# Performance work log

Measured on AMD Instinct MI355X. Metric: run time of the kernel, lower is better.

## Reference

```python
import jax, jax.numpy as jnp
import numpy as np

D_MODEL = 1024
NUM_HEADS = 16
DILATION = 2
SEG = 2048


def setup_inputs() -> dict:
    key = jax.random.key(0)
    k1, k2, k3, k4, k5 = jax.random.split(key, 5)
    B, S, D = 2, 8192, D_MODEL
    scale = 1.0 / np.sqrt(D)
    x = jax.random.normal(k1, (B, S, D), dtype=jnp.float32)
    wqkv = jax.random.normal(k2, (D, 3 * D), dtype=jnp.float32) * scale
    bqkv = jnp.zeros((3 * D,), dtype=jnp.float32)
    wo = jax.random.normal(k3, (D, D), dtype=jnp.float32) * scale
    bo = jnp.zeros((D,), dtype=jnp.float32)
    return {"x": x, "wqkv": wqkv, "bqkv": bqkv, "wo": wo, "bo": bo}


def reference(x, wqkv, bqkv, wo, bo):
    B, S, D = x.shape
    H = NUM_HEADS
    hd = D // H
    # segment reshape + dilated strided slice: [B, N, L, D]
    xs = x.reshape(B, -1, SEG, D)[:, :, ::DILATION, :]
    Bn, N, L, _ = xs.shape
    # fused QKV projection
    qkv = xs @ wqkv + bqkv                       # [B, N, L, 3D]
    q, k, v = jnp.split(qkv, 3, axis=-1)
    q = q.reshape(B, N, L, H, hd)
    k = k.reshape(B, N, L, H, hd)
    v = v.reshape(B, N, L, H, hd)
    scale = 1.0 / jnp.sqrt(jnp.asarray(hd, dtype=x.dtype))
    scores = jnp.einsum("bnqhd,bnkhd->bnhqk", q, k) * scale
    attn = jax.nn.softmax(scores, axis=-1)
    out = jnp.einsum("bnhqk,bnkhd->bnqhd", attn, v).reshape(B, N, L, D)
    out = out @ wo + bo                          # out projection
    return out.reshape(B, N * L, D)
```

## Files before the change

kernel.cpp:

```cpp
#include <hip/hip_runtime.h>
#include <hip/hip_bf16.h>
#include <stdint.h>

typedef __attribute__((ext_vector_type(8))) short short8;
typedef __attribute__((ext_vector_type(4))) float float4v;
typedef __attribute__((ext_vector_type(4))) unsigned int uint4v;
typedef unsigned short u16;

#if __has_builtin(__builtin_amdgcn_exp2f)
#define EXP2F(x) __builtin_amdgcn_exp2f(x)
#else
#define EXP2F(x) __expf(0.69314718056f * (x))
#endif

__device__ __forceinline__ u16 f2b(float f) {
    union { __hip_bfloat16 b; u16 u; } cv;
    cv.b = __float2bfloat16(f);
    return cv.u;
}

#define GLD16(g, l) __builtin_amdgcn_global_load_lds( \
    (const __attribute__((address_space(1))) void*)(g), \
    (__attribute__((address_space(3))) void*)(l), 16, 0, 0)

__global__ void convert_x(const float* __restrict__ x, u16* __restrict__ xb) {
    int id = blockIdx.x * 256 + threadIdx.x;
    int row = id >> 8;
    int c4 = id & 255;
    const float4* src = reinterpret_cast<const float4*>(x + (size_t)(2 * row) * 1024) + c4;
    float4 v = *src;
    ushort4 o;
    o.x = f2b(v.x); o.y = f2b(v.y); o.z = f2b(v.z); o.w = f2b(v.w);
    *(reinterpret_cast<ushort4*>(xb + (size_t)row * 1024) + c4) = o;
}

__global__ void transpose_convert(const float* __restrict__ in, u16* __restrict__ out,
                                  int K, int N) {
    __shared__ float tile[32][33];
    int n0 = blockIdx.x * 32, k0 = blockIdx.y * 32;
    int tx = threadIdx.x, ty = threadIdx.y;
#pragma unroll
    for (int i = 0; i < 4; i++)
        tile[ty + i * 8][tx] = in[(size_t)(k0 + ty + i * 8) * N + n0 + tx];
    __syncthreads();
#pragma unroll
    for (int i = 0; i < 4; i++)
        out[(size_t)(n0 + ty + i * 8) * K + k0 + tx] = f2b(tile[tx][ty + i * 8]);
}

template <int MODE>
__global__ __launch_bounds__(256) void gemm_bt(
    const u16* __restrict__ A, const u16* __restrict__ BT,
    const float* __restrict__ bias,
    float* __restrict__ Cf, u16* __restrict__ Cqk, u16* __restrict__ Cvt,
    int M, int N, int K) {
    __shared__ u16 As[128 * 64];
    __shared__ u16 Bs[128 * 64];
    const int tid = threadIdx.x;
    const int w = tid >> 6, l = tid & 63;
    const int q = l >> 4, c = l & 15;
    const int m0 = blockIdx.y * 128, n0 = blockIdx.x * 128;
    const int wm = (w >> 1) * 64, wn = (w & 1) * 64;

    const int srow = w * 8 + (l >> 3);
    const int scol = ((l & 7) ^ (srow & 7)) * 8;
    const u16* gA = A + (size_t)(m0 + srow) * K + scol;
    const u16* gB = BT + (size_t)(n0 + srow) * K + scol;
    char* AsB = (char*)&As[0];
    char* BsB = (char*)&Bs[0];
    const int ldsOff = (w * 8) * 128;

    float4v acc[4][4];
#pragma unroll
    for (int i = 0; i < 4; i++)
#pragma unroll
        for (int j = 0; j < 4; j++) acc[i][j] = {0.f, 0.f, 0.f, 0.f};

    const int cs = c & 7;

    for (int k0 = 0; k0 < K; k0 += 64) {
        __syncthreads();
#pragma unroll
        for (int j = 0; j < 4; j++) {
            GLD16(gA + (size_t)(j * 32) * K + k0, AsB + ldsOff + j * 32 * 128);
            GLD16(gB + (size_t)(j * 32) * K + k0, BsB + ldsOff + j * 32 * 128);
        }
        __syncthreads();
#pragma unroll
        for (int kk = 0; kk < 2; kk++) {
            const int phys = ((kk * 4 + q) ^ cs) * 8;
            short8 af[4], bf[4];
#pragma unroll
            for (int mt = 0; mt < 4; mt++)
                af[mt] = *reinterpret_cast<const short8*>(&As[(wm + mt * 16 + c) * 64 + phys]);
#pragma unroll
            for (int nt = 0; nt < 4; nt++)
                bf[nt] = *reinterpret_cast<const short8*>(&Bs[(wn + nt * 16 + c) * 64 + phys]);
#pragma unroll
            for (int mt = 0; mt < 4; mt++)
#pragma unroll
                for (int nt = 0; nt < 4; nt++)
                    acc[mt][nt] = __builtin_amdgcn_mfma_f32_16x16x32_bf16(af[mt], bf[nt], acc[mt][nt], 0, 0, 0);
        }
    }

    const int q4 = q * 4;
    if (MODE == 0) {
#pragma unroll
        for (int nt = 0; nt < 4; nt++) {
            int col = n0 + wn + nt * 16 + c;
            float bv = bias[col];
#pragma unroll
            for (int mt = 0; mt < 4; mt++) {
                int row = m0 + wm + mt * 16 + q4;
#pragma unroll
                for (int r = 0; r < 4; r++)
                    Cf[(size_t)(row + r) * N + col] = acc[mt][nt][r] + bv;
            }
        }
    } else {
        bool isV = (n0 + wn) >= 2048;
        float qscale = ((n0 + wn) < 1024) ? (0.125f * 1.44269504f) : 1.0f;
#pragma unroll
        for (int nt = 0; nt < 4; nt++) {
            int col = n0 + wn + nt * 16 + c;
            float bv = bias[col];
            if (!isV) {
#pragma unroll
                for (int mt = 0; mt < 4; mt++) {
                    int row = m0 + wm + mt * 16 + q4;
#pragma unroll
                    for (int r = 0; r < 4; r++)
                        Cqk[(size_t)(row + r) * 2048 + col] = f2b((acc[mt][nt][r] + bv) * qscale);
                }
            } else {
                int hd_ = col - 2048;
#pragma unroll
                for (int mt = 0; mt < 4; mt++) {
                    int row = m0 + wm + mt * 16 + q4;
                    int bn = row >> 10, key = row & 1023;
                    ushort4 pk;
                    pk.x = f2b(acc[mt][nt][0] + bv);
                    pk.y = f2b(acc[mt][nt][1] + bv);
                    pk.z = f2b(acc[mt][nt][2] + bv);
                    pk.w = f2b(acc[mt][nt][3] + bv);
                    *reinterpret_cast<ushort4*>(
                        &Cvt[((size_t)(bn << 10) + hd_) * 1024 + key]) = pk;
                }
            }
        }
    }
}

__global__ __launch_bounds__(256) void attn(const u16* __restrict__ qk,
                                            const u16* __restrict__ vt,
                                            u16* __restrict__ ob) {
    __shared__ u16 Ks[64 * 72];
    __shared__ u16 Vs[64 * 72];
    __shared__ u16 Ps[128 * 72];
    const int tid = threadIdx.x;
    const int w = tid >> 6, l = tid & 63, q = l >> 4, c = l & 15;
    const int combo = blockIdx.x, qtile = blockIdx.y;
    const int bn = combo >> 4, h = combo & 15;
    const int t0 = bn << 10;
    const int qoff = h << 6;
    const int koff = 1024 + (h << 6);
    const int vrow0 = combo << 6;
    const int qrow_base = t0 + qtile * 128 + w * 32;

    short8 v1;
    {
        u16 one = (c == 0) ? (u16)0x3F80 : (u16)0;
#pragma unroll
        for (int j = 0; j < 8; j++) v1[j] = (short)one;
    }

    short8 aq[2][2];
#pragma unroll
    for (int mt = 0; mt < 2; mt++)
#pragma unroll
        for (int ks = 0; ks < 2; ks++)
            aq[mt][ks] = *reinterpret_cast<const short8*>(
                qk + (size_t)(qrow_base + mt * 16 + c) * 2048 + qoff + ks * 32 + q * 8);

    float4v o_acc[2][4];
    float4v osum[2];
#pragma unroll
    for (int mt = 0; mt < 2; mt++) {
#pragma unroll
        for (int nt = 0; nt < 4; nt++) o_acc[mt][nt] = {0.f, 0.f, 0.f, 0.f};
        osum[mt] = {0.f, 0.f, 0.f, 0.f};
    }

    const int sr = tid >> 3;
    const int sc = (tid & 7) * 8;

    uint4v kreg[2], vreg[2];
#pragma unroll
    for (int i = 0; i < 2; i++) {
        int r = sr + i * 32;
        kreg[i] = *reinterpret_cast<const uint4v*>(
            qk + (size_t)(t0 + r) * 2048 + koff + sc);
        vreg[i] = *reinterpret_cast<const uint4v*>(
            vt + (size_t)(vrow0 + r) * 1024 + sc);
    }
#pragma unroll
    for (int i = 0; i < 2; i++) {
        int r = sr + i * 32;
        *reinterpret_cast<uint4v*>(&Ks[r * 72 + sc]) = kreg[i];
        *reinterpret_cast<uint4v*>(&Vs[r * 72 + sc]) = vreg[i];
    }
    __syncthreads();

    for (int chunk = 0; chunk < 16; chunk++) {
        if (chunk < 15) {
            const int key0n = (chunk + 1) * 64;
#pragma unroll
            for (int i = 0; i < 2; i++) {
                int r = sr + i * 32;
                kreg[i] = *reinterpret_cast<const uint4v*>(
                    qk + (size_t)(t0 + key0n + r) * 2048 + koff + sc);
                vreg[i] = *reinterpret_cast<const uint4v*>(
                    vt + (size_t)(vrow0 + r) * 1024 + key0n + sc);
            }
        }

        float4v s[2][4];
#pragma unroll
        for (int mt = 0; mt < 2; mt++)
#pragma unroll
            for (int nt = 0; nt < 4; nt++) s[mt][nt] = {0.f, 0.f, 0.f, 0.f};
#pragma unroll
        for (int ks = 0; ks < 2; ks++) {
            short8 bk[4];
#pragma unroll
            for (int nt = 0; nt < 4; nt++)
                bk[nt] = *reinterpret_cast<const short8*>(&Ks[(nt * 16 + c) * 72 + ks * 32 + q * 8]);
#pragma unroll
            for (int mt = 0; mt < 2; mt++)
#pragma unroll
                for (int nt = 0; nt < 4; nt++)
                    s[mt][nt] = __builtin_amdgcn_mfma_f32_16x16x32_bf16(aq[mt][ks], bk[nt], s[mt][nt], 0, 0, 0);
        }

#pragma unroll
        for (int mt = 0; mt < 2; mt++)
#pragma unroll
            for (int r = 0; r < 4; r++)
#pragma unroll
                for (int nt = 0; nt < 4; nt++)
                    Ps[(w * 32 + mt * 16 + q * 4 + r) * 72 + nt * 16 + c] =
                        f2b(EXP2F(s[mt][nt][r]));

#pragma unroll
        for (int ks = 0; ks < 2; ks++) {
            short8 pf[2], vf[4];
#pragma unroll
            for (int mt = 0; mt < 2; mt++)
                pf[mt] = *reinterpret_cast<const short8*>(
                    &Ps[(w * 32 + mt * 16 + c) * 72 + ks * 32 + q * 8]);
#pragma unroll
            for (int nt = 0; nt < 4; nt++)
                vf[nt] = *reinterpret_cast<const short8*>(&Vs[(nt * 16 + c) * 72 + ks * 32 + q * 8]);
#pragma unroll
            for (int mt = 0; mt < 2; mt++) {
#pragma unroll
                for (int nt = 0; nt < 4; nt++)
                    o_acc[mt][nt] = __builtin_amdgcn_mfma_f32_16x16x32_bf16(pf[mt], vf[nt], o_acc[mt][nt], 0, 0, 0);
                osum[mt] = __builtin_amdgcn_mfma_f32_16x16x32_bf16(pf[mt], v1, osum[mt], 0, 0, 0);
            }
        }

        if (chunk < 15) {
            __syncthreads();
#pragma unroll
            for (int i = 0; i < 2; i++) {
                int r = sr + i * 32;
                *reinterpret_cast<uint4v*>(&Ks[r * 72 + sc]) = kreg[i];
                *reinterpret_cast<uint4v*>(&Vs[r * 72 + sc]) = vreg[i];
            }
            __syncthreads();
        }
    }

#pragma unroll
    for (int mt = 0; mt < 2; mt++) {
        float inv[4];
#pragma unroll
        for (int r = 0; r < 4; r++) {
            float lv = __shfl(osum[mt][r], tid & 48);
            inv[r] = 1.0f / lv;
        }
#pragma unroll
        for (int nt = 0; nt < 4; nt++)
#pragma unroll
            for (int r = 0; r < 4; r++) {
                int row = qrow_base + mt * 16 + q * 4 + r;
                int col = (h << 6) + nt * 16 + c;
                ob[(size_t)row * 1024 + col] = f2b(o_acc[mt][nt][r] * inv[r]);
            }
    }
}

extern "C" void kernel_launch(void* const* d_in, const int* in_sizes, int n_in,
                              void* d_out, int out_size, void* d_ws, size_t ws_size,
                              hipStream_t stream) {
    const float* x    = (const float*)d_in[0];
    const float* wqkv = (const float*)d_in[1];
    const float* bqkv = (const float*)d_in[2];
    const float* wo   = (const float*)d_in[3];
    const float* bo   = (const float*)d_in[4];
    float* out = (float*)d_out;
    char* ws = (char*)d_ws;

    u16* xb    = (u16*)(ws);
    u16* wqkvT = (u16*)(ws + 16777216);
    u16* woT   = (u16*)(ws + 23068672);
    u16* qkb   = (u16*)(ws + 25165824);
    u16* vtb   = (u16*)(ws + 58720256);
    u16* obuf  = (u16*)(ws + 75497472);

    convert_x<<<8192, 256, 0, stream>>>(x, xb);
    transpose_convert<<<dim3(96, 32), dim3(32, 8), 0, stream>>>(wqkv, wqkvT, 1024, 3072);
    transpose_convert<<<dim3(32, 32), dim3(32, 8), 0, stream>>>(wo, woT, 1024, 1024);
    gemm_bt<1><<<dim3(24, 64), 256, 0, stream>>>(xb, wqkvT, bqkv,
                                                 nullptr, qkb, vtb, 8192, 3072, 1024);
    attn<<<dim3(128, 8), 256, 0, stream>>>(qkb, vtb, obuf);
    gemm_bt<0><<<dim3(8, 64), 256, 0, stream>>>(obuf, woT, bo,
                                                out, nullptr, nullptr, 8192, 1024, 1024);
}
```

Before: 260.1 us.

## Replace QKV GEMM with 256x256-tile 8-wave pipelined kernel

Adds a new QKV projection kernel that uses 256x256 output tiles with 512 threads and double-buffered LDS filled by direct global-to-LDS loads. The main loop is split into phases, each with barriers, priority raising and interleaved loads. This is meant to raise data reuse per tile and hide global-load latency behind the MFMA work. The cost is higher register and LDS use per block and fewer blocks in flight (384 instead of 1536), which risks lower occupancy and a tail effect.

```diff
diff --git a/kernel.cpp b/kernel.cpp
--- a/kernel.cpp
+++ b/kernel.cpp
@@ -147,6 +147,188 @@
                     *reinterpret_cast<ushort4*>(
                         &Cvt[((size_t)(bn << 10) + hd_) * 1024 + key]) = pk;
                 }
+            }
+        }
+    }
+}
+
+
+#define READ_A(BUF, MH) do {                                                     \
+    _Pragma("unroll") for (int mt = 0; mt < 4; mt++) {                           \
+        _Pragma("unroll") for (int ks = 0; ks < 2; ks++)                         \
+            af[mt][ks] = *reinterpret_cast<const short8*>(                       \
+                &As[BUF][(wm + (MH) * 64 + mt * 16 + c) * 64 + kc0 + ks * 32]);  \
+    }                                                                            \
+} while (0)
+
+#define READ_B(BUF, NH) do {                                                     \
+    _Pragma("unroll") for (int nt = 0; nt < 2; nt++) {                           \
+        _Pragma("unroll") for (int ks = 0; ks < 2; ks++)                         \
+            bf[NH][nt][ks] = *reinterpret_cast<const short8*>(                   \
+                &Bs[BUF][(wn + (NH) * 32 + nt * 16 + c) * 64 + kc0 + ks * 32]);  \
+    }                                                                            \
+} while (0)
+
+#define MFMA_Q(MH, NH) do {                                                      \
+    _Pragma("unroll") for (int mt = 0; mt < 4; mt++) {                           \
+        _Pragma("unroll") for (int nt = 0; nt < 2; nt++) {                       \
+            _Pragma("unroll") for (int ks = 0; ks < 2; ks++)                     \
+                acc[(MH) * 4 + mt][(NH) * 2 + nt] =                              \
+                    __builtin_amdgcn_mfma_f32_16x16x32_bf16(                     \
+                        af[mt][ks], bf[NH][nt][ks],                              \
+                        acc[(MH) * 4 + mt][(NH) * 2 + nt], 0, 0, 0);             \
+        }                                                                        \
+    }                                                                            \
+} while (0)
+
+#define PH_SYNC_MFMA(MH, NH) do {                                                \
+    __builtin_amdgcn_s_barrier();                                                \
+    asm volatile("s_waitcnt lgkmcnt(0)" ::: "memory");                           \
+    __builtin_amdgcn_sched_barrier(0);                                           \
+    __builtin_amdgcn_s_setprio(1);                                               \
+    MFMA_Q(MH, NH);                                                              \
+    __builtin_amdgcn_sched_barrier(0);                                           \
+    __builtin_amdgcn_s_setprio(0);                                               \
+    __builtin_amdgcn_s_barrier();                                                \
+} while (0)
+
+__global__ __launch_bounds__(512, 2) void gemm_qkv256(
+    const u16* __restrict__ A, const u16* __restrict__ BT,
+    const float* __restrict__ bias,
+    u16* __restrict__ Cqk, u16* __restrict__ Cvt,
+    int M, int N, int K) {
+    __shared__ u16 As[2][16384];
+    __shared__ u16 Bs[2][16384];
+    const int tid = threadIdx.x;
+    const int w = tid >> 6, l = tid & 63;
+    const int q = l >> 4, c = l & 15;
+    const int m0 = blockIdx.y * 256, n0 = blockIdx.x * 256;
+    const int wm = (w >> 2) * 128, wn = (w & 3) * 64;
+
+    const int rA = tid >> 3;
+    const int chS = ((tid & 7) ^ (((tid >> 5) & 1) << 1)) << 3;
+    const u16* gA = A + (size_t)(m0 + rA) * K + chS;
+    const u16* gB = BT + (size_t)(n0 + rA) * K + chS;
+    const int lbase = (w * 8) * 64;
+
+    auto issueA = [&](int buf, int kt, int h) {
+        const u16* g = gA + (size_t)(h * 128) * K + kt * 64;
+        u16* lp = &As[buf][h * 8192 + lbase];
+        GLD16(g, lp);
+        GLD16(g + (size_t)64 * K, lp + 4096);
+    };
+    auto issueB = [&](int buf, int kt, int h) {
+        const u16* g = gB + (size_t)(h * 128) * K + kt * 64;
+        u16* lp = &Bs[buf][h * 8192 + lbase];
+        GLD16(g, lp);
+        GLD16(g + (size_t)64 * K, lp + 4096);
+    };
+
+    const int sw2 = ((c >> 2) & 1) << 1;
+    const int kc0 = (q ^ sw2) << 3;
+
+    float4v acc[8][4];
+#pragma unroll
+    for (int i = 0; i < 8; i++)
+#pragma unroll
+        for (int j = 0; j < 4; j++) acc[i][j] = {0.f, 0.f, 0.f, 0.f};
+
+    short8 af[4][2];
+    short8 bf[2][2][2];
+
+    issueB(0, 0, 0); issueB(0, 0, 1); issueA(0, 0, 0); issueA(0, 0, 1);
+    issueB(1, 1, 0); issueB(1, 1, 1);
+    asm volatile("s_waitcnt vmcnt(4)" ::: "memory");
+    __builtin_amdgcn_s_barrier();
+
+    for (int it = 0; it < 7; ++it) {
+        const int t1 = 2 * it + 1, t2 = 2 * it + 2, t3 = 2 * it + 3;
+        READ_A(0, 0); READ_B(0, 0);
+        issueA(1, t1, 0);
+        PH_SYNC_MFMA(0, 0);
+
+        READ_B(0, 1);
+        issueA(1, t1, 1);
+        PH_SYNC_MFMA(0, 1);
+
+        READ_A(0, 1);
+        issueB(0, t2, 0);
+        PH_SYNC_MFMA(1, 1);
+
+        issueB(0, t2, 1);
+        asm volatile("s_waitcnt vmcnt(4)" ::: "memory");
+        PH_SYNC_MFMA(1, 0);
+
+        READ_A(1, 0); READ_B(1, 0);
+        issueA(0, t2, 0);
+        PH_SYNC_MFMA(0, 0);
+
+        READ_B(1, 1);
+        issueA(0, t2, 1);
+        PH_SYNC_MFMA(0, 1);
+
+        READ_A(1, 1);
+        issueB(1, t3, 0);
+        PH_SYNC_MFMA(1, 1);
+
+        issueB(1, t3, 1);
+        asm volatile("s_waitcnt vmcnt(4)" ::: "memory");
+        PH_SYNC_MFMA(1, 0);
+    }
+
+    READ_A(0, 0); READ_B(0, 0);
+    issueA(1, 15, 0);
+    PH_SYNC_MFMA(0, 0);
+
+    READ_B(0, 1);
+    issueA(1, 15, 1);
+    PH_SYNC_MFMA(0, 1);
+
+    READ_A(0, 1);
+    PH_SYNC_MFMA(1, 1);
+
+    asm volatile("s_waitcnt vmcnt(0)" ::: "memory");
+    PH_SYNC_MFMA(1, 0);
+
+    READ_A(1, 0); READ_B(1, 0);
+    PH_SYNC_MFMA(0, 0);
+
+    READ_B(1, 1);
+    PH_SYNC_MFMA(0, 1);
+
+    READ_A(1, 1);
+    PH_SYNC_MFMA(1, 1);
+
+    MFMA_Q(1, 0);
+
+    const bool isV = (n0 + wn) >= 2048;
+    const float qscale = ((n0 + wn) < 1024) ? (0.125f * 1.44269504f) : 1.0f;
+    const int q4 = q * 4;
+#pragma unroll
+    for (int ni = 0; ni < 4; ni++) {
+        int col = n0 + wn + ni * 16 + c;
+        float bv = bias[col];
+        if (!isV) {
+#pragma unroll
+            for (int mi = 0; mi < 8; mi++) {
+                int row = m0 + wm + mi * 16 + q4;
+#pragma unroll
+                for (int r = 0; r < 4; r++)
+                    Cqk[(size_t)(row + r) * 2048 + col] = f2b((acc[mi][ni][r] + bv) * qscale);
+            }
+        } else {
+            int hd_ = col - 2048;
+#pragma unroll
+            for (int mi = 0; mi < 8; mi++) {
+                int row = m0 + wm + mi * 16 + q4;
+                int bn = row >> 10, key = row & 1023;
+                ushort4 pk;
+                pk.x = f2b(acc[mi][ni][0] + bv);
+                pk.y = f2b(acc[mi][ni][1] + bv);
+                pk.z = f2b(acc[mi][ni][2] + bv);
+                pk.w = f2b(acc[mi][ni][3] + bv);
+                *reinterpret_cast<ushort4*>(
+                    &Cvt[((size_t)(bn << 10) + hd_) * 1024 + key]) = pk;
             }
         }
     }
@@ -323,8 +505,8 @@
     convert_x<<<8192, 256, 0, stream>>>(x, xb);
     transpose_convert<<<dim3(96, 32), dim3(32, 8), 0, stream>>>(wqkv, wqkvT, 1024, 3072);
     transpose_convert<<<dim3(32, 32), dim3(32, 8), 0, stream>>>(wo, woT, 1024, 1024);
-    gemm_bt<1><<<dim3(24, 64), 256, 0, stream>>>(xb, wqkvT, bqkv,
-                                                 nullptr, qkb, vtb, 8192, 3072, 1024);
+    gemm_qkv256<<<dim3(12, 32), 512, 0, stream>>>(xb, wqkvT, bqkv,
+                                                  qkb, vtb, 8192, 3072, 1024);
     attn<<<dim3(128, 8), 256, 0, stream>>>(qkb, vtb, obuf);
     gemm_bt<0><<<dim3(8, 64), 256, 0, stream>>>(obuf, woT, bo,
                                                 out, nullptr, nullptr, 8192, 1024, 1024);
```

Result: slower. 281.3 us (+8.1%).
